# Optimization experiments

Measured on AMD Instinct MI355X. Metric: run time of the kernel, lower is better.

The kernel has to match this reference:

```python
import jax, jax.numpy as jnp
import numpy as np

B, S, D, H, FF = 2, 2048, 1024, 16, 4096
DK = D // H
LOCAL_WINDOW, STRIDE = 128, 128
NEG = -1000000000.0
EPS = 1e-5


def _layernorm(x, g, b):
    mu = jnp.mean(x, axis=-1, keepdims=True)
    var = jnp.mean(jnp.square(x - mu), axis=-1, keepdims=True)
    return (x - mu) * jax.lax.rsqrt(var + EPS) * g + b


def _strided_mask(seq):
    # allowed(i, j): j <= i and (i-j <= local_window or (i-j) % stride == 0)
    i = jnp.arange(seq)[:, None]
    j = jnp.arange(seq)[None, :]
    d = i - j
    return (d >= 0) & ((d <= LOCAL_WINDOW) | (d % STRIDE == 0))  # [S, S] bool


def setup_inputs() -> dict:
    key = jax.random.key(0)
    ks = jax.random.split(key, 18)
    w = lambda k, shape: jax.random.normal(k, shape, jnp.float32) * 0.02
    return {
        "x": jax.random.normal(ks[0], (B, S, D), jnp.float32),
        "mask": jnp.ones((1, 1, S, S), jnp.int32),
        "Wq": w(ks[1], (D, D)), "bq": jnp.zeros((D,), jnp.float32),
        "Wk": w(ks[2], (D, D)), "bk": jnp.zeros((D,), jnp.float32),
        "Wv": w(ks[3], (D, D)), "bv": jnp.zeros((D,), jnp.float32),
        "Wo": w(ks[4], (D, D)), "bo": jnp.zeros((D,), jnp.float32),
        "W1": w(ks[5], (D, FF)), "bf1": jnp.zeros((FF,), jnp.float32),
        "W2": w(ks[6], (FF, D)), "bf2": jnp.zeros((D,), jnp.float32),
        "g1": jnp.ones((D,), jnp.float32), "bl1": jnp.zeros((D,), jnp.float32),
        "g2": jnp.ones((D,), jnp.float32), "bl2": jnp.zeros((D,), jnp.float32),
    }


def reference(x, mask, Wq, bq, Wk, bk, Wv, bv, Wo, bo,
              W1, bf1, W2, bf2, g1, bl1, g2, bl2):
    b, s, d = x.shape
    sm = _strided_mask(s)[None, None]  # [1,1,S,S]

    # pre-LN self-attention
    n = _layernorm(x, g1, bl1)
    split = lambda t: t.reshape(b, s, H, DK).transpose(0, 2, 1, 3)  # [B,H,S,DK]
    q = split(n @ Wq + bq)
    k = split(n @ Wk + bk)
    v = split(n @ Wv + bv)

    scores = jnp.einsum('bhqd,bhkd->bhqk', q, k) / jnp.sqrt(jnp.float32(DK))
    scores = jnp.where(sm, scores, NEG)          # strided/local mask
    scores = jnp.where(mask == 0, NEG, scores)   # user mask
    attn = jax.nn.softmax(scores, axis=-1)
    o = jnp.einsum('bhqk,bhkd->bhqd', attn, v)
    o = o.transpose(0, 2, 1, 3).reshape(b, s, d) @ Wo + bo
    x = x + o

    # pre-LN FFN (GELU exact, matching torch nn.GELU default)
    n2 = _layernorm(x, g2, bl2)
    ff = jax.nn.gelu(n2 @ W1 + bf1, approximate=False) @ W2 + bf2
    return x + ff
```

## Files before the change

### kernel.cpp

```cpp
#include <hip/hip_runtime.h>
#include <math.h>

typedef unsigned int u32;
typedef unsigned short u16;

#define B_  2
#define S_  2048
#define D_  1024
#define H_  16
#define DK_ 64
#define FF_ 4096
#define NEG_ -1000000000.0f

typedef __attribute__((ext_vector_type(8))) short short8;
typedef __attribute__((ext_vector_type(4))) float floatx4;
typedef __attribute__((ext_vector_type(4))) unsigned short ushort4_t;

__device__ inline u16 f2b(float f) {
    union { float f; u32 u; } v; v.f = f;
    u32 r = (v.u + 0x7fffu + ((v.u >> 16) & 1u)) >> 16;
    return (u16)r;
}
__device__ inline float b2f(u16 b) {
    union { u32 u; float f; } v; v.u = ((u32)b) << 16;
    return v.f;
}

__device__ inline void gl_lds16(const u16* g, u16* l) {
    __builtin_amdgcn_global_load_lds((const __attribute__((address_space(1))) u32*)g,
                                     (__attribute__((address_space(3))) u32*)l, 16, 0, 0);
}

__global__ void tconv4(const float* __restrict__ W0, const float* __restrict__ W1_,
                       const float* __restrict__ W2_, const float* __restrict__ W3,
                       u16* __restrict__ dstBase) {
    __shared__ float tile[32][33];
    int z = blockIdx.z;
    const float* Wm = (z == 0) ? W0 : (z == 1) ? W1_ : (z == 2) ? W2_ : W3;
    u16* Wt = dstBase + (size_t)z * 1024 * 1024;
    const int K = 1024, N = 1024;
    int n0 = blockIdx.x * 32, k0 = blockIdx.y * 32;
    int tx = threadIdx.x & 31, ty = threadIdx.x >> 5;
#pragma unroll
    for (int r = 0; r < 32; r += 8)
        tile[ty + r][tx] = Wm[(size_t)(k0 + ty + r) * N + n0 + tx];
    __syncthreads();
#pragma unroll
    for (int r = 0; r < 32; r += 8)
        Wt[(size_t)(n0 + ty + r) * K + k0 + tx] = f2b(tile[tx][ty + r]);
}

__global__ void tconv(const float* __restrict__ Wm, u16* __restrict__ Wt, int K, int N) {
    __shared__ float tile[32][33];
    int n0 = blockIdx.x * 32, k0 = blockIdx.y * 32;
    int tx = threadIdx.x & 31, ty = threadIdx.x >> 5;
#pragma unroll
    for (int r = 0; r < 32; r += 8)
        tile[ty + r][tx] = Wm[(size_t)(k0 + ty + r) * N + n0 + tx];
    __syncthreads();
#pragma unroll
    for (int r = 0; r < 32; r += 8)
        Wt[(size_t)(n0 + ty + r) * K + k0 + tx] = f2b(tile[tx][ty + r]);
}

__global__ void catbias(const float* __restrict__ bq, const float* __restrict__ bk,
                        const float* __restrict__ bv, float* __restrict__ out) {
    int i = blockIdx.x * 256 + threadIdx.x;
    float v = (i < 1024) ? bq[i] : (i < 2048) ? bk[i - 1024] : bv[i - 2048];
    out[i] = v;
}

__global__ __launch_bounds__(256)
void mask_tiles(const int* __restrict__ mask, int* __restrict__ tflag) {
    int jt = blockIdx.x, it = blockIdx.y;
    const int* base = mask + (size_t)it * 128 * S_ + jt * 128;
    int t = threadIdx.x;
    int ok = 1;
    for (int e = t; e < 128 * 32; e += 256) {
        int r = e >> 5, c4 = e & 31;
        int4 vv = *(const int4*)&base[(size_t)r * S_ + c4 * 4];
        ok &= (vv.x != 0) & (vv.y != 0) & (vv.z != 0) & (vv.w != 0);
    }
    ok = (int)__all(ok);
    __shared__ int red[4];
    if ((t & 63) == 0) red[t >> 6] = ok;
    __syncthreads();
    if (t == 0) tflag[it * 16 + jt] = red[0] & red[1] & red[2] & red[3];
}

__global__ void ln_bf16(const float* __restrict__ x, const float* __restrict__ g,
                        const float* __restrict__ b, u16* __restrict__ out) {
    int row = blockIdx.x;
    int t = threadIdx.x;
    const float* xr = x + (size_t)row * D_;
    __shared__ float red[256];

    float v[4];
    float s = 0.f;
#pragma unroll
    for (int i = 0; i < 4; i++) { v[i] = xr[i * 256 + t]; s += v[i]; }
    red[t] = s; __syncthreads();
    for (int off = 128; off > 0; off >>= 1) {
        if (t < off) red[t] += red[t + off];
        __syncthreads();
    }
    float mu = red[0] * (1.0f / D_);
    __syncthreads();

    float vs = 0.f;
#pragma unroll
    for (int i = 0; i < 4; i++) { float d = v[i] - mu; vs += d * d; }
    red[t] = vs; __syncthreads();
    for (int off = 128; off > 0; off >>= 1) {
        if (t < off) red[t] += red[t + off];
        __syncthreads();
    }
    float rstd = rsqrtf(red[0] * (1.0f / D_) + 1e-5f);

    u16* outr = out + (size_t)row * D_;
#pragma unroll
    for (int i = 0; i < 4; i++) {
        int col = i * 256 + t;
        outr[col] = f2b((v[i] - mu) * rstd * g[col] + b[col]);
    }
}

__global__ __launch_bounds__(256)
void merge_ln(const u16* __restrict__ P, const float* __restrict__ x,
              const float* __restrict__ bo, const float* __restrict__ g,
              const float* __restrict__ bl, float* __restrict__ x1,
              u16* __restrict__ n2) {
    const size_t MN = (size_t)B_ * S_ * D_;
    int row = blockIdx.x, t = threadIdx.x;
    size_t base = (size_t)row * D_;
    __shared__ float red[256];

    float v[4];
    float s = 0.f;
#pragma unroll
    for (int i = 0; i < 4; i++) {
        int col = i * 256 + t;
        float val = x[base + col] + bo[col] + b2f(P[base + col]) + b2f(P[MN + base + col]);
        v[i] = val; s += val;
    }
    red[t] = s; __syncthreads();
    for (int off = 128; off > 0; off >>= 1) {
        if (t < off) red[t] += red[t + off];
        __syncthreads();
    }
    float mu = red[0] * (1.0f / D_);
    __syncthreads();

    float vs = 0.f;
#pragma unroll
    for (int i = 0; i < 4; i++) { float d = v[i] - mu; vs += d * d; }
    red[t] = vs; __syncthreads();
    for (int off = 128; off > 0; off >>= 1) {
        if (t < off) red[t] += red[t + off];
        __syncthreads();
    }
    float rstd = rsqrtf(red[0] * (1.0f / D_) + 1e-5f);

#pragma unroll
    for (int i = 0; i < 4; i++) {
        int col = i * 256 + t;
        x1[base + col] = v[i];
        n2[base + col] = f2b((v[i] - mu) * rstd * g[col] + bl[col]);
    }
}

template <int EPI>
__global__ __launch_bounds__(256, 4)
void gemm_bt(const u16* __restrict__ A, const u16* __restrict__ Bt,
             const float* __restrict__ bias, const float* __restrict__ R,
             void* __restrict__ Cv, int M, int N, int K, int ldA, int ldB) {
    __shared__ u16 As[2][128 * 32];
    __shared__ u16 Bs[2][128 * 32];
    int tid = threadIdx.x;
    int lane = tid & 63, w = tid >> 6;
    int wm = w >> 1, wn = w & 1;
    int m0 = blockIdx.x * 128, n0 = blockIdx.y * 128;
    size_t koff = (size_t)blockIdx.z * K;

    floatx4 acc[4][4];
#pragma unroll
    for (int a = 0; a < 4; a++)
#pragma unroll
        for (int b2 = 0; b2 < 4; b2++) acc[a][b2] = (floatx4){0.f, 0.f, 0.f, 0.f};

    int r4 = lane >> 2;
    int qg = ((lane & 3) ^ ((lane >> 3) & 3)) * 8;
    const u16* Ag0 = A + (size_t)(m0 + w * 16 + r4) * ldA + koff + qg;
    const u16* Bg0 = Bt + (size_t)(n0 + w * 16 + r4) * ldB + koff + qg;
    const int ldsOff = (w * 16) * 32;

    int c = lane & 15, g = lane >> 4;
    int sw = (g ^ ((c >> 1) & 3)) * 8;

    const int nIter = K >> 5;

    gl_lds16(Ag0, &As[0][ldsOff]);
    gl_lds16(Ag0 + (size_t)64 * ldA, &As[0][ldsOff + 64 * 32]);
    gl_lds16(Bg0, &Bs[0][ldsOff]);
    gl_lds16(Bg0 + (size_t)64 * ldB, &Bs[0][ldsOff + 64 * 32]);

    for (int it = 0; it < nIter; it++) {
        __syncthreads();
        int cur = it & 1, nxt = cur ^ 1;
        if (it + 1 < nIter) {
            int kk = (it + 1) << 5;
            gl_lds16(Ag0 + kk, &As[nxt][ldsOff]);
            gl_lds16(Ag0 + kk + (size_t)64 * ldA, &As[nxt][ldsOff + 64 * 32]);
            gl_lds16(Bg0 + kk, &Bs[nxt][ldsOff]);
            gl_lds16(Bg0 + kk + (size_t)64 * ldB, &Bs[nxt][ldsOff + 64 * 32]);
        }
        short8 fa[4], fb[4];
#pragma unroll
        for (int a = 0; a < 4; a++)
            fa[a] = *(const short8*)&As[cur][(wm * 64 + a * 16 + c) * 32 + sw];
#pragma unroll
        for (int b2 = 0; b2 < 4; b2++)
            fb[b2] = *(const short8*)&Bs[cur][(wn * 64 + b2 * 16 + c) * 32 + sw];
#pragma unroll
        for (int a = 0; a < 4; a++)
#pragma unroll
            for (int b2 = 0; b2 < 4; b2++)
                acc[a][b2] = __builtin_amdgcn_mfma_f32_16x16x32_bf16(fa[a], fb[b2], acc[a][b2], 0, 0, 0);
    }

    int mb = m0 + wm * 64, nb = n0 + wn * 64;
#pragma unroll
    for (int a = 0; a < 4; a++) {
#pragma unroll
        for (int b2 = 0; b2 < 4; b2++) {
            int mrow = mb + a * 16 + g * 4;
            int ncol = nb + b2 * 16 + c;
            float bv = (EPI == 3) ? 0.f : bias[ncol];
#pragma unroll
            for (int r = 0; r < 4; r++) {
                int m = mrow + r;
                float vvv = acc[a][b2][r] + bv;
                if (EPI == 0) {
                    int which = ncol >> 10, col = ncol & 1023;
                    if (which == 0) vvv *= 0.125f;
                    int bb = m >> 11, ss = m & 2047, hh = col >> 6, dk = col & 63;
                    ((u16*)Cv)[(size_t)which * ((size_t)B_ * S_ * D_) +
                               ((((size_t)bb * H_ + hh) * S_) + ss) * DK_ + dk] = f2b(vvv);
                } else if (EPI == 1) {
                    ((float*)Cv)[(size_t)m * N + ncol] = vvv + R[(size_t)m * N + ncol];
                } else if (EPI == 2) {
                    float u = 0.79788456080286536f * fmaf(0.044715f * vvv, vvv * vvv, vvv);
                    float th = 1.f - 2.f / (1.f + __expf(2.f * u));
                    ((u16*)Cv)[(size_t)m * N + ncol] = f2b(0.5f * vvv * (1.f + th));
                } else {
                    ((u16*)Cv)[(size_t)blockIdx.z * M * N + (size_t)m * N + ncol] = f2b(vvv);
                }
            }
        }
    }
}

__global__ __launch_bounds__(256)
void ffn2_merge(const u16* __restrict__ P, const float* __restrict__ x1,
                const float* __restrict__ bf2, float* __restrict__ out) {
    const size_t MN = (size_t)B_ * S_ * D_;
    int e = (blockIdx.x * 256 + threadIdx.x) * 4;
    float4 xv = *(const float4*)&x1[e];
    float4 bv = *(const float4*)&bf2[e & 1023];
    float o0 = xv.x + bv.x, o1 = xv.y + bv.y, o2 = xv.z + bv.z, o3 = xv.w + bv.w;
#pragma unroll
    for (int z = 0; z < 4; z++) {
        ushort4_t pv = *(const ushort4_t*)&P[z * MN + e];
        o0 += b2f(pv[0]); o1 += b2f(pv[1]); o2 += b2f(pv[2]); o3 += b2f(pv[3]);
    }
    *(float4*)&out[e] = (float4){o0, o1, o2, o3};
}

#define MAXB_ 14
__global__ __launch_bounds__(256)
void attn4(const u16* __restrict__ q, const u16* __restrict__ k,
           const u16* __restrict__ v, const int* __restrict__ mask,
           const int* __restrict__ tileOK, u16* __restrict__ ob) {
    __shared__ u16 sh[19456];
    u16* Kw = sh;
    u16* Qs = sh + 13824;
    u16* Vh = sh + 12800;

    const int bh = blockIdx.x;
    const int i0 = (31 - blockIdx.y) * 64;
    const int b  = bh >> 4, h = bh & 15;
    const int t  = threadIdx.x;
    const int lane = t & 63, w = t >> 6;
    const int c = lane & 15, g = lane >> 4;
    const int g4 = g * 4;
    const int qloc16 = w * 16;

    const u16* qg = q + ((size_t)bh * S_ + i0) * DK_;
    const u16* kg = k + (size_t)bh * S_ * DK_;
    const u16* vg = v + (size_t)bh * S_ * DK_;

    const int wlo = (i0 >= 128) ? i0 - 128 : 0;
    const int wn  = i0 + 64 - wlo;
    const int nb  = (i0 >= 256) ? (i0 >> 7) - 1 : 0;
    const int jb0 = i0 & 127;
    const int dd0 = i0 - wlo;

    bool allOK = true;
    {
        const int* rowf = tileOK + (i0 >> 7) * 16;
        int jt0 = wlo >> 7, jt1 = (i0 + 63) >> 7;
        for (int jt = jt0; jt <= jt1; jt++) allOK &= (rowf[jt] != 0);
        for (int m = 0; m < nb; m++) allOK &= (rowf[m] != 0);
    }

    for (int e = t; e < 64 * 8; e += 256) {
        int row = e >> 3, dc = e & 7;
        *(short8*)&Qs[row * 72 + dc * 8] = *(const short8*)(qg + row * 64 + dc * 8);
    }
    for (int e = t; e < wn * 8; e += 256) {
        int row = e >> 3, dc = e & 7;
        *(short8*)&Kw[row * 72 + dc * 8] = *(const short8*)(kg + (size_t)(wlo + row) * 64 + dc * 8);
    }
    __syncthreads();

    float sbr[MAXB_];
    {
        short8 qv0 = *(const short8*)&Qs[(qloc16 + c) * 72 + g * 8];
        short8 qv1 = *(const short8*)&Qs[(qloc16 + c) * 72 + 32 + g * 8];
#pragma unroll
        for (int m = 0; m < MAXB_; m++) {
            sbr[m] = NEG_;
            if (m < nb) {
                int jrow = jb0 + (m << 7) + qloc16 + c;
                short8 kv0 = *(const short8*)(kg + (size_t)jrow * 64 + g * 8);
                short8 kv1 = *(const short8*)(kg + (size_t)jrow * 64 + 32 + g * 8);
                float p = 0.f;
#pragma unroll
                for (int i = 0; i < 8; i++) {
                    p += b2f((u16)qv0[i]) * b2f((u16)kv0[i]);
                    p += b2f((u16)qv1[i]) * b2f((u16)kv1[i]);
                }
                p += __shfl_xor(p, 16);
                p += __shfl_xor(p, 32);
                if (!allOK && mask[(size_t)(i0 + qloc16 + c) * S_ + jrow] == 0) p = NEG_;
                sbr[m] = p;
            }
        }
    }

    floatx4 sc[12];
#pragma unroll
    for (int ct = 0; ct < 12; ct++) sc[ct] = (floatx4){0.f, 0.f, 0.f, 0.f};
    {
        short8 fa0 = *(const short8*)&Qs[(qloc16 + c) * 72 + g * 8];
        short8 fa1 = *(const short8*)&Qs[(qloc16 + c) * 72 + 32 + g * 8];
#pragma unroll
        for (int ct = 0; ct < 12; ct++) {
            short8 fb0 = *(const short8*)&Kw[(ct * 16 + c) * 72 + g * 8];
            short8 fb1 = *(const short8*)&Kw[(ct * 16 + c) * 72 + 32 + g * 8];
            sc[ct] = __builtin_amdgcn_mfma_f32_16x16x32_bf16(fa0, fb0, sc[ct], 0, 0, 0);
            sc[ct] = __builtin_amdgcn_mfma_f32_16x16x32_bf16(fa1, fb1, sc[ct], 0, 0, 0);
        }
    }

#pragma unroll
    for (int ct = 0; ct < 12; ct++) {
        int cidx = ct * 16 + c;
        int j = wlo + cidx;
#pragma unroll
        for (int r = 0; r < 4; r++) {
            int qloc = qloc16 + g4 + r;
            int d = dd0 + qloc - cidx;
            bool ok = (d >= 0) && (d <= 128);
            if (ok && !allOK) ok = (mask[(size_t)(i0 + qloc) * S_ + j] != 0);
            sc[ct][r] = ok ? sc[ct][r] : NEG_;
        }
    }

    float mv[4], inv[4];
#pragma unroll
    for (int r = 0; r < 4; r++) {
        float bs[MAXB_];
#pragma unroll
        for (int m = 0; m < MAXB_; m++)
            bs[m] = (m < nb) ? __shfl(sbr[m], g4 + r, 64) : NEG_;
        float mm = -1e30f;
#pragma unroll
        for (int ct = 0; ct < 12; ct++) mm = fmaxf(mm, sc[ct][r]);
        mm = fmaxf(mm, __shfl_xor(mm, 1));
        mm = fmaxf(mm, __shfl_xor(mm, 2));
        mm = fmaxf(mm, __shfl_xor(mm, 4));
        mm = fmaxf(mm, __shfl_xor(mm, 8));
#pragma unroll
        for (int m = 0; m < MAXB_; m++)
            if (m < nb) mm = fmaxf(mm, bs[m]);
        float sum = 0.f;
#pragma unroll
        for (int ct = 0; ct < 12; ct++) {
            float e = __expf(sc[ct][r] - mm);
            sc[ct][r] = e;
            sum += e;
        }
        sum += __shfl_xor(sum, 1);
        sum += __shfl_xor(sum, 2);
        sum += __shfl_xor(sum, 4);
        sum += __shfl_xor(sum, 8);
#pragma unroll
        for (int m = 0; m < MAXB_; m++)
            if (m < nb) sum += __expf(bs[m] - mm);
        mv[r] = mm;
        inv[r] = 1.f / sum;
    }

    __syncthreads();
    u16* P = Kw;
#pragma unroll
    for (int ct = 0; ct < 12; ct++)
#pragma unroll
        for (int r = 0; r < 4; r++)
            P[(qloc16 + g4 + r) * 200 + ct * 16 + c] = f2b(sc[ct][r]);

    for (int e = t; e < 768; e += 256) {
        int dc = e / 96, jl = e - dc * 96;
        short8 val = {0, 0, 0, 0, 0, 0, 0, 0};
        if (jl < wn) val = *(const short8*)(vg + (size_t)(wlo + jl) * 64 + dc * 8);
#pragma unroll
        for (int i = 0; i < 8; i++) Vh[(dc * 8 + i) * 104 + jl] = (u16)val[i];
    }
    __syncthreads();

    floatx4 o[4];
#pragma unroll
    for (int nt = 0; nt < 4; nt++) o[nt] = (floatx4){0.f, 0.f, 0.f, 0.f};
#pragma unroll
    for (int ks = 0; ks < 3; ks++) {
        short8 pa = *(const short8*)&P[(qloc16 + c) * 200 + ks * 32 + g * 8];
#pragma unroll
        for (int nt = 0; nt < 4; nt++) {
            short8 vb = *(const short8*)&Vh[(nt * 16 + c) * 104 + ks * 32 + g * 8];
            o[nt] = __builtin_amdgcn_mfma_f32_16x16x32_bf16(pa, vb, o[nt], 0, 0, 0);
        }
    }

    if (wn > 96) {
        __syncthreads();
        for (int e = t; e < 768; e += 256) {
            int dc = e / 96, jl = e - dc * 96;
            int j2 = 96 + jl;
            short8 val = {0, 0, 0, 0, 0, 0, 0, 0};
            if (j2 < wn) val = *(const short8*)(vg + (size_t)(wlo + j2) * 64 + dc * 8);
#pragma unroll
            for (int i = 0; i < 8; i++) Vh[(dc * 8 + i) * 104 + jl] = (u16)val[i];
        }
        __syncthreads();
#pragma unroll
        for (int ks = 0; ks < 3; ks++) {
            short8 pa = *(const short8*)&P[(qloc16 + c) * 200 + 96 + ks * 32 + g * 8];
#pragma unroll
            for (int nt = 0; nt < 4; nt++) {
                short8 vb = *(const short8*)&Vh[(nt * 16 + c) * 104 + ks * 32 + g * 8];
                o[nt] = __builtin_amdgcn_mfma_f32_16x16x32_bf16(pa, vb, o[nt], 0, 0, 0);
            }
        }
    }

#pragma unroll
    for (int m = 0; m < MAXB_; m++) {
        if (m < nb) {
            int vbase = jb0 + (m << 7) + qloc16 + g4;
            u16 vv[4][4];
#pragma unroll
            for (int r = 0; r < 4; r++)
#pragma unroll
                for (int nt = 0; nt < 4; nt++)
                    vv[r][nt] = vg[(size_t)(vbase + r) * 64 + nt * 16 + c];
#pragma unroll
            for (int r = 0; r < 4; r++) {
                float bs = __shfl(sbr[m], g4 + r, 64);
                float pb = __expf(bs - mv[r]);
#pragma unroll
                for (int nt = 0; nt < 4; nt++)
                    o[nt][r] += pb * b2f(vv[r][nt]);
            }
        }
    }

#pragma unroll
    for (int nt = 0; nt < 4; nt++) {
#pragma unroll
        for (int r = 0; r < 4; r++) {
            int qi = i0 + qloc16 + g4 + r;
            ob[((size_t)b * S_ + qi) * D_ + h * 64 + nt * 16 + c] = f2b(o[nt][r] * inv[r]);
        }
    }
}

extern "C" void kernel_launch(void* const* d_in, const int* in_sizes, int n_in,
                              void* d_out, int out_size, void* d_ws, size_t ws_size,
                              hipStream_t stream) {
    const float* x    = (const float*)d_in[0];
    const int*   mask = (const int*)  d_in[1];
    const float* Wq   = (const float*)d_in[2];
    const float* bq   = (const float*)d_in[3];
    const float* Wk   = (const float*)d_in[4];
    const float* bk   = (const float*)d_in[5];
    const float* Wv   = (const float*)d_in[6];
    const float* bv   = (const float*)d_in[7];
    const float* Wo   = (const float*)d_in[8];
    const float* bo   = (const float*)d_in[9];
    const float* W1   = (const float*)d_in[10];
    const float* bf1  = (const float*)d_in[11];
    const float* W2   = (const float*)d_in[12];
    const float* bf2  = (const float*)d_in[13];
    const float* g1   = (const float*)d_in[14];
    const float* bl1  = (const float*)d_in[15];
    const float* g2   = (const float*)d_in[16];
    const float* bl2  = (const float*)d_in[17];

    char* wsb = (char*)d_ws;
    const size_t MB = 1024 * 1024;
    u16*   WtQKV  = (u16*)(wsb + 0);
    u16*   WtO    = (u16*)(wsb + 6 * MB);
    u16*   Wt1    = (u16*)(wsb + 8 * MB);
    u16*   Wt2    = (u16*)(wsb + 16 * MB);
    u16*   n1b    = (u16*)(wsb + 24 * MB);
    u16*   qkv    = (u16*)(wsb + 32 * MB);
    u16*   obb    = (u16*)(wsb + 56 * MB);
    float* x1     = (float*)(wsb + 32 * MB);
    u16*   ff1b   = (u16*)(wsb + 48 * MB);
    u16*   Ppart  = (u16*)(wsb + 82 * MB);
    u16*   PpartO = (u16*)(wsb + 82 * MB);
    float* bcat   = (float*)(wsb + 114 * MB);
    int*   tflag  = (int*)(wsb + 115 * MB);
    u16*   n2b    = n1b;

    const int M = B_ * S_;
    const size_t SZ = (size_t)B_ * S_ * D_;

    mask_tiles<<<dim3(16, 16), 256, 0, stream>>>(mask, tflag);
    tconv4<<<dim3(32, 32, 4), 256, 0, stream>>>(Wq, Wk, Wv, Wo, WtQKV);
    tconv<<<dim3(128, 32), 256, 0, stream>>>(W1, Wt1, 1024, 4096);
    tconv<<<dim3(32, 128), 256, 0, stream>>>(W2, Wt2, 4096, 1024);
    catbias<<<12, 256, 0, stream>>>(bq, bk, bv, bcat);

    ln_bf16<<<M, 256, 0, stream>>>(x, g1, bl1, n1b);

    gemm_bt<0><<<dim3(32, 24), 256, 0, stream>>>(n1b, WtQKV, bcat, nullptr, qkv,
                                                 M, 3072, 1024, 1024, 1024);

    attn4<<<dim3(32, 32), 256, 0, stream>>>(qkv, qkv + SZ, qkv + 2 * SZ, mask, tflag, obb);

    gemm_bt<3><<<dim3(32, 8, 2), 256, 0, stream>>>(obb, WtO, nullptr, nullptr, PpartO,
                                                   M, 1024, 512, 1024, 1024);
    merge_ln<<<M, 256, 0, stream>>>(PpartO, x, bo, g2, bl2, x1, n2b);

    gemm_bt<2><<<dim3(32, 32), 256, 0, stream>>>(n2b, Wt1, bf1, nullptr, ff1b,
                                                 M, 4096, 1024, 1024, 1024);

    gemm_bt<3><<<dim3(32, 8, 4), 256, 0, stream>>>(ff1b, Wt2, nullptr, nullptr, Ppart,
                                                   M, 1024, 1024, 4096, 4096);
    ffn2_merge<<<(int)(SZ / 1024), 256, 0, stream>>>(Ppart, x1, bf2, (float*)d_out);
}
```

Baseline: 371.5 us.

## Replace 128x128 GEMM with 256x256 8-wave ping-pong pipelined GEMM

Replaces the 4-wave 128x128 bf16 MFMA GEMM with an 8-wave 256x256 tile kernel. It uses 128KB of XOR-swizzled LDS with K-step 64 double buffering, and interleaves direct-to-LDS global loads with quadrant MFMA groups separated by barriers and setprio. It also remaps workgroup IDs across XCDs and drops the unused residual epilogue. The intent is higher arithmetic intensity and better overlap of loads with MFMA. The cost is fewer workgroups (e.g. 192 for QKV, 128 for O-proj), which risks underfilling the 256 CUs, plus many barriers per iteration.

```diff
diff --git a/kernel.cpp b/kernel.cpp
--- a/kernel.cpp
+++ b/kernel.cpp
@@ -169,95 +169,160 @@
     }
 }
 
+#define BARR asm volatile("s_barrier" ::: "memory")
+#define WAITL0 do { asm volatile("s_waitcnt lgkmcnt(0)" ::: "memory"); \
+                    __builtin_amdgcn_sched_barrier(0); } while (0)
+
 template <int EPI>
-__global__ __launch_bounds__(256, 4)
-void gemm_bt(const u16* __restrict__ A, const u16* __restrict__ Bt,
-             const float* __restrict__ bias, const float* __restrict__ R,
-             void* __restrict__ Cv, int M, int N, int K, int ldA, int ldB) {
-    __shared__ u16 As[2][128 * 32];
-    __shared__ u16 Bs[2][128 * 32];
-    int tid = threadIdx.x;
-    int lane = tid & 63, w = tid >> 6;
-    int wm = w >> 1, wn = w & 1;
-    int m0 = blockIdx.x * 128, n0 = blockIdx.y * 128;
+__global__ __launch_bounds__(512, 2)
+void gemm8(const u16* __restrict__ A, const u16* __restrict__ Bt,
+           const float* __restrict__ bias, void* __restrict__ Cv,
+           int M, int N, int K, int ldA, int ldB) {
+    __shared__ u16 sh2[65536];
+    const int tid = threadIdx.x;
+    const int lane = tid & 63, w = tid >> 6;
+    const int wm = w >> 2, wn = w & 3;
+    const int c = lane & 15, g = lane >> 4;
+    const int cbase = c * 128 + g * 16;
+    const int xo = (c & 7) << 4;
+
+    int nMt = gridDim.x;
+    int nwg = gridDim.x * gridDim.y;
+    int id = blockIdx.x + nMt * blockIdx.y;
+    int qq = nwg >> 3;
+    int sid = (id & 7) * qq + (id >> 3);
+    int m0 = (sid % nMt) * 256, n0 = (sid / nMt) * 256;
     size_t koff = (size_t)blockIdx.z * K;
 
-    floatx4 acc[4][4];
-#pragma unroll
-    for (int a = 0; a < 4; a++)
-#pragma unroll
-        for (int b2 = 0; b2 < 4; b2++) acc[a][b2] = (floatx4){0.f, 0.f, 0.f, 0.f};
-
-    int r4 = lane >> 2;
-    int qg = ((lane & 3) ^ ((lane >> 3) & 3)) * 8;
-    const u16* Ag0 = A + (size_t)(m0 + w * 16 + r4) * ldA + koff + qg;
-    const u16* Bg0 = Bt + (size_t)(n0 + w * 16 + r4) * ldB + koff + qg;
-    const int ldsOff = (w * 16) * 32;
-
-    int c = lane & 15, g = lane >> 4;
-    int sw = (g ^ ((c >> 1) & 3)) * 8;
-
-    const int nIter = K >> 5;
-
-    gl_lds16(Ag0, &As[0][ldsOff]);
-    gl_lds16(Ag0 + (size_t)64 * ldA, &As[0][ldsOff + 64 * 32]);
-    gl_lds16(Bg0, &Bs[0][ldsOff]);
-    gl_lds16(Bg0 + (size_t)64 * ldB, &Bs[0][ldsOff + 64 * 32]);
-
-    for (int it = 0; it < nIter; it++) {
-        __syncthreads();
-        int cur = it & 1, nxt = cur ^ 1;
-        if (it + 1 < nIter) {
-            int kk = (it + 1) << 5;
-            gl_lds16(Ag0 + kk, &As[nxt][ldsOff]);
-            gl_lds16(Ag0 + kk + (size_t)64 * ldA, &As[nxt][ldsOff + 64 * 32]);
-            gl_lds16(Bg0 + kk, &Bs[nxt][ldsOff]);
-            gl_lds16(Bg0 + kk + (size_t)64 * ldB, &Bs[nxt][ldsOff + 64 * 32]);
-        }
-        short8 fa[4], fb[4];
-#pragma unroll
-        for (int a = 0; a < 4; a++)
-            fa[a] = *(const short8*)&As[cur][(wm * 64 + a * 16 + c) * 32 + sw];
-#pragma unroll
-        for (int b2 = 0; b2 < 4; b2++)
-            fb[b2] = *(const short8*)&Bs[cur][(wn * 64 + b2 * 16 + c) * 32 + sw];
-#pragma unroll
-        for (int a = 0; a < 4; a++)
-#pragma unroll
-            for (int b2 = 0; b2 < 4; b2++)
-                acc[a][b2] = __builtin_amdgcn_mfma_f32_16x16x32_bf16(fa[a], fb[b2], acc[a][b2], 0, 0, 0);
-    }
-
-    int mb = m0 + wm * 64, nb = n0 + wn * 64;
-#pragma unroll
-    for (int a = 0; a < 4; a++) {
-#pragma unroll
-        for (int b2 = 0; b2 < 4; b2++) {
-            int mrow = mb + a * 16 + g * 4;
-            int ncol = nb + b2 * 16 + c;
-            float bv = (EPI == 3) ? 0.f : bias[ncol];
-#pragma unroll
-            for (int r = 0; r < 4; r++) {
-                int m = mrow + r;
-                float vvv = acc[a][b2][r] + bv;
-                if (EPI == 0) {
-                    int which = ncol >> 10, col = ncol & 1023;
-                    if (which == 0) vvv *= 0.125f;
-                    int bb = m >> 11, ss = m & 2047, hh = col >> 6, dk = col & 63;
-                    ((u16*)Cv)[(size_t)which * ((size_t)B_ * S_ * D_) +
-                               ((((size_t)bb * H_ + hh) * S_) + ss) * DK_ + dk] = f2b(vvv);
-                } else if (EPI == 1) {
-                    ((float*)Cv)[(size_t)m * N + ncol] = vvv + R[(size_t)m * N + ncol];
-                } else if (EPI == 2) {
-                    float u = 0.79788456080286536f * fmaf(0.044715f * vvv, vvv * vvv, vvv);
-                    float th = 1.f - 2.f / (1.f + __expf(2.f * u));
-                    ((u16*)Cv)[(size_t)m * N + ncol] = f2b(0.5f * vvv * (1.f + th));
-                } else {
-                    ((u16*)Cv)[(size_t)blockIdx.z * M * N + (size_t)m * N + ncol] = f2b(vvv);
+    const int nT = K >> 6, nI = nT >> 1;
+
+    const int sr = tid >> 3;
+    const int sk = ((tid & 7) * 8) ^ (((tid >> 3) & 7) << 3);
+    const u16* gA0 = A + (size_t)(m0 + sr) * ldA + koff + sk;
+    const u16* gB0 = Bt + (size_t)(n0 + sr) * ldB + koff + sk;
+    const int dst0 = w * 512;
+
+#define STG_A(t_, h_) do { \
+    const u16* s_ = gA0 + (size_t)(h_) * 128 * ldA + (t_) * 64; \
+    u16* l_ = &sh2[((((t_) & 1) * 2 + (h_)) * 8192) + dst0]; \
+    gl_lds16(s_, l_); \
+    gl_lds16(s_ + (size_t)64 * ldA, l_ + 4096); \
+} while (0)
+#define STG_B(t_, h_) do { \
+    const u16* s_ = gB0 + (size_t)(h_) * 128 * ldB + (t_) * 64; \
+    u16* l_ = &sh2[32768 + ((((t_) & 1) * 2 + (h_)) * 8192) + dst0]; \
+    gl_lds16(s_, l_); \
+    gl_lds16(s_ + (size_t)64 * ldB, l_ + 4096); \
+} while (0)
+
+    short8 fa[8], fb0[4], fb1[4];
+    floatx4 acc[2][2][4][2];
+#pragma unroll
+    for (int i = 0; i < 2; i++)
+#pragma unroll
+        for (int j = 0; j < 2; j++)
+#pragma unroll
+            for (int a = 0; a < 4; a++)
+#pragma unroll
+                for (int b2 = 0; b2 < 2; b2++)
+                    acc[i][j][a][b2] = (floatx4){0.f, 0.f, 0.f, 0.f};
+
+#define DS_A(d_, qr_) do { \
+    int rb_ = ((d_) * 2 + wm) * 16384; \
+    _Pragma("unroll") for (int a_ = 0; a_ < 4; a_++) \
+    _Pragma("unroll") for (int k_ = 0; k_ < 2; k_++) { \
+        int lin_ = (qr_) * 8192 + a_ * 2048 + cbase + k_ * 64; \
+        fa[a_ * 2 + k_] = *(const short8*)((const char*)sh2 + rb_ + (lin_ ^ xo)); } \
+} while (0)
+#define DS_B(d_, qc_, fb_) do { \
+    int rb_ = 65536 + ((d_) * 2 + (wn >> 1)) * 16384; \
+    _Pragma("unroll") for (int b_ = 0; b_ < 2; b_++) \
+    _Pragma("unroll") for (int k_ = 0; k_ < 2; k_++) { \
+        int lin_ = (wn & 1) * 8192 + (qc_) * 4096 + b_ * 2048 + cbase + k_ * 64; \
+        fb_[b_ * 2 + k_] = *(const short8*)((const char*)sh2 + rb_ + (lin_ ^ xo)); } \
+} while (0)
+#define MFMA16(qr_, qc_, fb_) do { \
+    __builtin_amdgcn_s_setprio(1); \
+    _Pragma("unroll") for (int a_ = 0; a_ < 4; a_++) \
+    _Pragma("unroll") for (int b_ = 0; b_ < 2; b_++) \
+    _Pragma("unroll") for (int k_ = 0; k_ < 2; k_++) \
+        acc[qr_][qc_][a_][b_] = __builtin_amdgcn_mfma_f32_16x16x32_bf16( \
+            fa[a_ * 2 + k_], fb_[b_ * 2 + k_], acc[qr_][qc_][a_][b_], 0, 0, 0); \
+    __builtin_amdgcn_s_setprio(0); \
+} while (0)
+
+    STG_B(0, 0); STG_B(0, 1); STG_A(0, 0); STG_A(0, 1);
+    STG_A(1, 0); STG_A(1, 1);
+    asm volatile("s_waitcnt vmcnt(4)" ::: "memory");
+    BARR;
+
+    for (int it2 = 0; it2 < nI; it2++) {
+        const int t1 = 2 * it2 + 1, tn0 = t1 + 1, tn1 = t1 + 2;
+        DS_A(0, 0); DS_B(0, 0, fb0);
+        STG_B(t1, 0);
+        BARR; WAITL0; MFMA16(0, 0, fb0); BARR;
+        DS_B(0, 1, fb1);
+        STG_B(t1, 1);
+        BARR; WAITL0; MFMA16(0, 1, fb1); BARR;
+        DS_A(0, 1);
+        if (tn0 < nT) STG_B(tn0, 0);
+        BARR; WAITL0; MFMA16(1, 1, fb1); BARR;
+        if (tn0 < nT) {
+            STG_B(tn0, 1);
+            asm volatile("s_waitcnt vmcnt(4)" ::: "memory");
+        } else {
+            asm volatile("s_waitcnt vmcnt(0)" ::: "memory");
+        }
+        BARR; WAITL0; MFMA16(1, 0, fb0); BARR;
+        DS_A(1, 0); DS_B(1, 0, fb0);
+        if (tn0 < nT) STG_A(tn0, 0);
+        BARR; WAITL0; MFMA16(0, 0, fb0); BARR;
+        DS_B(1, 1, fb1);
+        if (tn0 < nT) STG_A(tn0, 1);
+        BARR; WAITL0; MFMA16(0, 1, fb1); BARR;
+        DS_A(1, 1);
+        if (tn1 < nT) STG_A(tn1, 0);
+        BARR; WAITL0; MFMA16(1, 1, fb1); BARR;
+        if (tn1 < nT) STG_A(tn1, 1);
+        if (it2 + 1 < nI) asm volatile("s_waitcnt vmcnt(4)" ::: "memory");
+        BARR; WAITL0; MFMA16(1, 0, fb0); BARR;
+    }
+
+#pragma unroll
+    for (int qr = 0; qr < 2; qr++)
+#pragma unroll
+        for (int qc = 0; qc < 2; qc++)
+#pragma unroll
+            for (int a = 0; a < 4; a++)
+#pragma unroll
+                for (int b2 = 0; b2 < 2; b2++) {
+                    int mrow = m0 + wm * 128 + qr * 64 + a * 16 + g * 4;
+                    int ncol = n0 + wn * 64 + qc * 32 + b2 * 16 + c;
+                    float bv = (EPI == 3) ? 0.f : bias[ncol];
+#pragma unroll
+                    for (int r = 0; r < 4; r++) {
+                        int m = mrow + r;
+                        float vvv = acc[qr][qc][a][b2][r] + bv;
+                        if (EPI == 0) {
+                            int which = ncol >> 10, col = ncol & 1023;
+                            if (which == 0) vvv *= 0.125f;
+                            int bb = m >> 11, ss = m & 2047, hh = col >> 6, dk = col & 63;
+                            ((u16*)Cv)[(size_t)which * ((size_t)B_ * S_ * D_) +
+                                       ((((size_t)bb * H_ + hh) * S_) + ss) * DK_ + dk] = f2b(vvv);
+                        } else if (EPI == 2) {
+                            float u = 0.79788456080286536f * fmaf(0.044715f * vvv, vvv * vvv, vvv);
+                            float th = 1.f - 2.f / (1.f + __expf(2.f * u));
+                            ((u16*)Cv)[(size_t)m * N + ncol] = f2b(0.5f * vvv * (1.f + th));
+                        } else {
+                            ((u16*)Cv)[(size_t)blockIdx.z * M * N + (size_t)m * N + ncol] = f2b(vvv);
+                        }
+                    }
                 }
-            }
-        }
-    }
+#undef STG_A
+#undef STG_B
+#undef DS_A
+#undef DS_B
+#undef MFMA16
 }
 
 __global__ __launch_bounds__(256)
@@ -545,19 +610,19 @@
 
     ln_bf16<<<M, 256, 0, stream>>>(x, g1, bl1, n1b);
 
-    gemm_bt<0><<<dim3(32, 24), 256, 0, stream>>>(n1b, WtQKV, bcat, nullptr, qkv,
-                                                 M, 3072, 1024, 1024, 1024);
+    gemm8<0><<<dim3(16, 12, 1), 512, 0, stream>>>(n1b, WtQKV, bcat, qkv,
+                                                  M, 3072, 1024, 1024, 1024);
 
     attn4<<<dim3(32, 32), 256, 0, stream>>>(qkv, qkv + SZ, qkv + 2 * SZ, mask, tflag, obb);
 
-    gemm_bt<3><<<dim3(32, 8, 2), 256, 0, stream>>>(obb, WtO, nullptr, nullptr, PpartO,
-                                                   M, 1024, 512, 1024, 1024);
+    gemm8<3><<<dim3(16, 4, 2), 512, 0, stream>>>(obb, WtO, nullptr, PpartO,
+                                                 M, 1024, 512, 1024, 1024);
     merge_ln<<<M, 256, 0, stream>>>(PpartO, x, bo, g2, bl2, x1, n2b);
 
-    gemm_bt<2><<<dim3(32, 32), 256, 0, stream>>>(n2b, Wt1, bf1, nullptr, ff1b,
-                                                 M, 4096, 1024, 1024, 1024);
-
-    gemm_bt<3><<<dim3(32, 8, 4), 256, 0, stream>>>(ff1b, Wt2, nullptr, nullptr, Ppart,
-                                                   M, 1024, 1024, 4096, 4096);
+    gemm8<2><<<dim3(16, 16, 1), 512, 0, stream>>>(n2b, Wt1, bf1, ff1b,
+                                                  M, 4096, 1024, 1024, 1024);
+
+    gemm8<3><<<dim3(16, 4, 4), 512, 0, stream>>>(ff1b, Wt2, nullptr, Ppart,
+                                                 M, 1024, 1024, 4096, 4096);
     ffn2_merge<<<(int)(SZ / 1024), 256, 0, stream>>>(Ppart, x1, bf2, (float*)d_out);
 }
```

Measured after the change: 371.9 us. No clear change (+0.1%).
